# Performance work log

Hardware: AMD Instinct MI355X
Metric: run time of the kernel (lower is better)

Reference implementation:

```python
import jax, jax.numpy as jnp
import numpy as np

NEG = -1e30   # log-space 'zero' (avoid -inf arithmetic)
EPS = 1e-7    # keras.backend.epsilon()


def setup_inputs() -> dict:
    key = jax.random.key(0)
    k1, k2 = jax.random.split(key)
    B, T, C, L = 512, 512, 128, 64
    logits = jax.random.normal(k1, (B, T, C), dtype=jnp.float32)
    # ctc_batch_cost expects softmax posteriors (it takes log(y_pred + eps) itself)
    y_pred = jax.nn.softmax(logits, axis=-1)
    # blank index is C-1 (TF CTC convention), so labels live in [0, C-2]
    y_true = jax.random.randint(k2, (B, L), 0, C - 1, dtype=jnp.int32)
    return {"y_true": y_true, "y_pred": y_pred}


def _ctc_loss(y_true, y_pred):
    """Faithful jax port of keras.backend.ctc_batch_cost as invoked by CTCLayer:
    input_length = y_pred.shape[2] (source bug, replicated), label_length = L,
    blank = num_classes - 1, standard merge-repeated CTC alpha recursion."""
    B, T, C = y_pred.shape
    L = y_true.shape[1]
    input_len = C                     # source uses tf.shape(y_pred)[2]
    blank = C - 1
    logp = jnp.log(y_pred[:, :input_len, :] + EPS)        # [B, Tu, C]

    S = 2 * L + 1                                        # extended label length
    ext = jnp.full((B, S), blank, dtype=jnp.int32).at[:, 1::2].set(
        y_true.astype(jnp.int32))                        # blank-interleaved labels
    # gather per-state log-probs: lp[b, t, s] = logp[b, t, ext[b, s]]
    lp = jnp.take_along_axis(
        logp, jnp.broadcast_to(ext[:, None, :], (B, input_len, S)), axis=2)

    # s-2 skip allowed when ext[s] != blank and ext[s] != ext[s-2]
    skip_ok = jnp.concatenate(
        [jnp.zeros((B, 2), dtype=bool),
         (ext[:, 2:] != blank) & (ext[:, 2:] != ext[:, :-2])], axis=1)

    neg1 = jnp.full((B, 1), NEG, dtype=logp.dtype)
    neg2 = jnp.full((B, 2), NEG, dtype=logp.dtype)

    def lse3(a, b, c):
        m = jnp.maximum(jnp.maximum(jnp.maximum(a, b), c), NEG)
        return m + jnp.log(jnp.exp(a - m) + jnp.exp(b - m) + jnp.exp(c - m))

    def step(alpha, lp_t):
        a1 = jnp.concatenate([neg1, alpha[:, :-1]], axis=1)
        a2 = jnp.where(skip_ok,
                       jnp.concatenate([neg2, alpha[:, :-2]], axis=1), NEG)
        return lse3(alpha, a1, a2) + lp_t, None

    alpha0 = (jnp.full((B, S), NEG, dtype=logp.dtype)
              .at[:, 0].set(lp[:, 0, 0])
              .at[:, 1].set(lp[:, 0, 1]))
    alphaT, _ = jax.lax.scan(step, alpha0, jnp.swapaxes(lp, 0, 1)[1:])

    tail = jnp.stack([alphaT[:, S - 2], alphaT[:, S - 1]], axis=1)
    loss = -jax.scipy.special.logsumexp(tail, axis=1)
    return loss[:, None]                                 # [B, 1], as ctc_batch_cost


def reference(y_true, y_pred):
    return _ctc_loss(y_true, y_pred)
```

## Files before the change

kernel.cpp:

```cpp
#include <hip/hip_runtime.h>


#define BB 512
#define TT 512
#define CC 128
#define LL 64
#define TU 128
#define EPSF 1e-7f
#define PD 16
#define LN2F 0.69314718055994530942f
#define NWAVE 8

template <int CTRL>
__device__ __forceinline__ float dpp_f(float x) {
    const int xi = __float_as_int(x);
    return __int_as_float(__builtin_amdgcn_update_dpp(xi, xi, CTRL, 0xF, 0xF, false));
}

__device__ __forceinline__ float shift_up1z(float x) {
    const int xi = __float_as_int(x);
    return __int_as_float(__builtin_amdgcn_update_dpp(xi, xi, 0x138 ,
                                                      0xF, 0xF, true));
}

__device__ __forceinline__ float wave_max(float v) {
    v = fmaxf(v, dpp_f<0xB1>(v));
    v = fmaxf(v, dpp_f<0x4E>(v));
    v = fmaxf(v, dpp_f<0x141>(v));
    v = fmaxf(v, dpp_f<0x140>(v));
    v = fmaxf(v, dpp_f<0x142>(v));
    v = fmaxf(v, dpp_f<0x143>(v));
    return __int_as_float(__builtin_amdgcn_readlane(__float_as_int(v), 63));
}

__device__ __forceinline__ void renorm(float& b0, float& b1, float& b2,
                                       int& acc, int lane, int t_done) {
    float m = fmaxf(b0, b1);
    if (lane == 63) m = fmaxf(m, b2);
    m = (lane + 64 >= t_done) ? m : 0.0f;
    const float M = wave_max(m);
    int e = 0;
    (void)frexpf(M, &e);
    const float scale = ldexpf(1.0f, -e);
    b0 *= scale; b1 *= scale; b2 *= scale;
    acc += e;
}

__global__ __launch_bounds__(NWAVE * 64) void ctc_wave(const int* __restrict__ y_true,
                                                       const float* __restrict__ y_pred,
                                                       float* __restrict__ out) {
    __shared__ float lds[TU * CC];
    const int b = blockIdx.x;
    const int tid = threadIdx.x;
    const int wid = tid >> 6;
    const int lane = tid & 63;
    const float* yp = y_pred + (size_t)b * TT * CC;

    {
        auto ldsb = (__attribute__((address_space(3))) unsigned int*)lds;
        auto gb   = (const __attribute__((address_space(1))) unsigned int*)yp;
#pragma unroll
        for (int r = 0; r < 64 / NWAVE; ++r) {
            const int i = wid * (64 / NWAVE) + r;
            __builtin_amdgcn_global_load_lds(gb + i * 256 + lane * 4,
                                             ldsb + i * 256, 16, 0, 0);
        }
    }
    asm volatile("s_waitcnt vmcnt(0)" ::: "memory");
    __syncthreads();
    if (wid != 0) return;

    const int lbl  = y_true[b * LL + lane];
    const int lblp = __shfl_up(lbl, 1);
    const float skipf = (lane >= 1 && lbl != lblp) ? 1.0f : 0.0f;

    const float pbr0e = lds[lane * CC + (CC - 1)] + EPSF;
    const float pbr1e = lds[(64 + lane) * CC + (CC - 1)] + EPSF;

    float plr[PD];
#pragma unroll
    for (int j = 0; j < PD; ++j) plr[j] = lds[(1 + j) * CC + lbl];

    const float pl0 = lds[lbl] + EPSF;
    const float pb0 = __int_as_float(__builtin_amdgcn_readlane(__float_as_int(pbr0e), 0));
    float b0 = (lane == 0) ? pb0 : 0.0f;
    float b1 = (lane == 0) ? pl0 : 0.0f;
    float b2 = 0.0f;
    int acc = 0;

#pragma unroll
    for (int t = 1; t < TU; ++t) {
        const int slot = (t - 1) & (PD - 1);
        const float plv = plr[slot];
        const int trow = (t + PD < TU) ? (t + PD) : (TU - 1);
        plr[slot] = lds[trow * CC + lbl];
        const float ple = plv + EPSF;
        const float pbe = __int_as_float(__builtin_amdgcn_readlane(
            __float_as_int((t < 64) ? pbr0e : pbr1e), t & 63));
        const float b1p = shift_up1z(b1);
        const float nb0 = (b0 + b1p) * pbe;
        const float h   = __builtin_fmaf(skipf, b1p, b1);
        const float nb1 = (b0 + h) * ple;
        const float nb2 = (b2 + b1) * pbe;
        b0 = nb0; b1 = nb1; b2 = nb2;
        if ((t & 7) == 0) renorm(b0, b1, b2, acc, lane, t);
    }

    if (lane == 63) {
        const float s = b1 + b2;
        out[b] = -LN2F * (__log2f(s) + (float)acc);
    }
}

extern "C" void kernel_launch(void* const* d_in, const int* in_sizes, int n_in,
                              void* d_out, int out_size, void* d_ws, size_t ws_size,
                              hipStream_t stream) {
    const int*   y_true = (const int*)d_in[0];
    const float* y_pred = (const float*)d_in[1];
    float*       out    = (float*)d_out;
    (void)in_sizes; (void)n_in; (void)out_size; (void)d_ws; (void)ws_size;

    ctc_wave<<<BB, NWAVE * 64, 0, stream>>>(y_true, y_pred, out);
}
```

Measured before the change: 11.45 us.

## Overlap chunked global-to-LDS loads with the CTC recursion in wave 0

The y_pred slab is now loaded in eight time-ordered chunks of sixteen rows. Wave 0 starts the alpha recursion on each chunk as soon as it arrives, waiting on staged vmcnt counts and a barrier per chunk, rather than waiting for the whole tile first. This hides load latency behind serial compute. In exchange, all waves must stay alive to join every barrier, and the per-chunk LDS gathers replace the old deep register prefetch.

```diff
diff --git a/kernel.cpp b/kernel.cpp
--- a/kernel.cpp
+++ b/kernel.cpp
@@ -7,9 +7,10 @@
 #define LL 64
 #define TU 128
 #define EPSF 1e-7f
-#define PD 16
 #define LN2F 0.69314718055994530942f
 #define NWAVE 8
+#define NCHUNK 8
+#define CROWS 16
 
 template <int CTRL>
 __device__ __forceinline__ float dpp_f(float x) {
@@ -56,57 +57,69 @@
     const int lane = tid & 63;
     const float* yp = y_pred + (size_t)b * TT * CC;
 
+    const int lbl = y_true[b * LL + lane];
+
     {
         auto ldsb = (__attribute__((address_space(3))) unsigned int*)lds;
         auto gb   = (const __attribute__((address_space(1))) unsigned int*)yp;
 #pragma unroll
-        for (int r = 0; r < 64 / NWAVE; ++r) {
-            const int i = wid * (64 / NWAVE) + r;
-            __builtin_amdgcn_global_load_lds(gb + i * 256 + lane * 4,
-                                             ldsb + i * 256, 16, 0, 0);
+        for (int c = 0; c < NCHUNK; ++c) {
+            __builtin_amdgcn_global_load_lds(gb + c * 2048 + wid * 256 + lane * 4,
+                                             ldsb + c * 2048 + wid * 256, 16, 0, 0);
         }
     }
-    asm volatile("s_waitcnt vmcnt(0)" ::: "memory");
-    __syncthreads();
-    if (wid != 0) return;
 
-    const int lbl  = y_true[b * LL + lane];
     const int lblp = __shfl_up(lbl, 1);
     const float skipf = (lane >= 1 && lbl != lblp) ? 1.0f : 0.0f;
 
-    const float pbr0e = lds[lane * CC + (CC - 1)] + EPSF;
-    const float pbr1e = lds[(64 + lane) * CC + (CC - 1)] + EPSF;
-
-    float plr[PD];
-#pragma unroll
-    for (int j = 0; j < PD; ++j) plr[j] = lds[(1 + j) * CC + lbl];
-
-    const float pl0 = lds[lbl] + EPSF;
-    const float pb0 = __int_as_float(__builtin_amdgcn_readlane(__float_as_int(pbr0e), 0));
-    float b0 = (lane == 0) ? pb0 : 0.0f;
-    float b1 = (lane == 0) ? pl0 : 0.0f;
-    float b2 = 0.0f;
+    float b0 = 0.0f, b1 = 0.0f, b2 = 0.0f;
     int acc = 0;
 
-#pragma unroll
-    for (int t = 1; t < TU; ++t) {
-        const int slot = (t - 1) & (PD - 1);
-        const float plv = plr[slot];
-        const int trow = (t + PD < TU) ? (t + PD) : (TU - 1);
-        plr[slot] = lds[trow * CC + lbl];
-        const float ple = plv + EPSF;
-        const float pbe = __int_as_float(__builtin_amdgcn_readlane(
-            __float_as_int((t < 64) ? pbr0e : pbr1e), t & 63));
-        const float b1p = shift_up1z(b1);
-        const float nb0 = (b0 + b1p) * pbe;
-        const float h   = __builtin_fmaf(skipf, b1p, b1);
-        const float nb1 = (b0 + h) * ple;
-        const float nb2 = (b2 + b1) * pbe;
-        b0 = nb0; b1 = nb1; b2 = nb2;
-        if ((t & 7) == 0) renorm(b0, b1, b2, acc, lane, t);
+#define CHUNK_BODY(c_)                                                          \
+    {                                                                           \
+        asm volatile("s_waitcnt vmcnt(%0)" :: "i"(NCHUNK - 1 - (c_)) : "memory"); \
+        __builtin_amdgcn_s_barrier();                                           \
+        if (wid == 0) {                                                         \
+            const float pbce =                                                  \
+                lds[((c_) * CROWS + (lane & 15)) * CC + (CC - 1)] + EPSF;       \
+            float plc[CROWS];                                                   \
+            _Pragma("unroll")                                                   \
+            for (int j = 0; j < CROWS; ++j)                                     \
+                plc[j] = lds[((c_) * CROWS + j) * CC + lbl];                    \
+            _Pragma("unroll")                                                   \
+            for (int j = 0; j < CROWS; ++j) {                                   \
+                const int t = (c_) * CROWS + j;                                 \
+                const float pbe = __int_as_float(                               \
+                    __builtin_amdgcn_readlane(__float_as_int(pbce), j));        \
+                if (t == 0) {                                                   \
+                    b0 = (lane == 0) ? pbe : 0.0f;                              \
+                    b1 = (lane == 0) ? (plc[0] + EPSF) : 0.0f;                  \
+                    b2 = 0.0f;                                                  \
+                } else {                                                        \
+                    const float ple = plc[j] + EPSF;                            \
+                    const float b1p = shift_up1z(b1);                           \
+                    const float nb0 = (b0 + b1p) * pbe;                         \
+                    const float h   = __builtin_fmaf(skipf, b1p, b1);           \
+                    const float nb1 = (b0 + h) * ple;                           \
+                    const float nb2 = (b2 + b1) * pbe;                          \
+                    b0 = nb0; b1 = nb1; b2 = nb2;                               \
+                    if ((t & 7) == 0) renorm(b0, b1, b2, acc, lane, t);         \
+                }                                                               \
+            }                                                                   \
+        }                                                                       \
     }
 
-    if (lane == 63) {
+    CHUNK_BODY(0)
+    CHUNK_BODY(1)
+    CHUNK_BODY(2)
+    CHUNK_BODY(3)
+    CHUNK_BODY(4)
+    CHUNK_BODY(5)
+    CHUNK_BODY(6)
+    CHUNK_BODY(7)
+#undef CHUNK_BODY
+
+    if (wid == 0 && lane == 63) {
         const float s = b1 + b2;
         out[b] = -LN2F * (__log2f(s) + (float)acc);
     }
```

After: 11.98 us. 1.05x slower.
